# Kernel tuning notes

Hardware: AMD Instinct MI355X
Metric: run time of the kernel (lower is better)

Reference implementation:

```python
import jax, jax.numpy as jnp
import numpy as np

LN_EPS = 1e-5

def _ln(x, g, b):
    m = x.mean(-1, keepdims=True)
    v = jnp.mean((x - m) ** 2, axis=-1, keepdims=True)
    return (x - m) * jax.lax.rsqrt(v + LN_EPS) * g + b


def setup_inputs() -> dict:
    key = jax.random.key(0)
    ks = jax.random.split(key, 8)
    B, S, H = 8, 4096, 2048
    V, L, E = 32, 8, 64   # vocab_size, symbol seq_len, embedding_dim
    sc = 0.02
    d = {}
    d["hidden_states"] = jax.random.normal(ks[0], (B, S, H), jnp.float32)
    # uniform in (0,1) for Gumbel noise: g = -log(-log(u))
    d["gumbel_u"] = jax.random.uniform(ks[1], (B, L, V), jnp.float32, 1e-6, 1.0 - 1e-6)
    d["enc_w1"] = jax.random.normal(ks[2], (256, H), jnp.float32) * sc
    d["enc_b1"] = jnp.zeros((256,), jnp.float32)
    d["ln1_g"] = jnp.ones((256,), jnp.float32)
    d["ln1_b"] = jnp.zeros((256,), jnp.float32)
    d["enc_w2"] = jax.random.normal(ks[3], (L * V, 256), jnp.float32) * sc
    d["enc_b2"] = jnp.zeros((L * V,), jnp.float32)
    d["embed"] = jax.random.normal(ks[4], (V, E), jnp.float32) * sc
    d["dec_w1"] = jax.random.normal(ks[5], (256, L * E), jnp.float32) * sc
    d["dec_b1"] = jnp.zeros((256,), jnp.float32)
    d["ln2_g"] = jnp.ones((256,), jnp.float32)
    d["ln2_b"] = jnp.zeros((256,), jnp.float32)
    d["dec_w2"] = jax.random.normal(ks[6], (H, 256), jnp.float32) * sc
    d["dec_b2"] = jnp.zeros((H,), jnp.float32)
    return d


def reference(hidden_states, gumbel_u, enc_w1, enc_b1, ln1_g, ln1_b, enc_w2, enc_b2,
              embed, dec_w1, dec_b1, ln2_g, ln2_b, dec_w2, dec_b2):
    V, L, TAU = 32, 8, 1.0
    B, S, H = hidden_states.shape
    E = embed.shape[1]
    # encode: mean-pool over sequence, then MLP -> logits [B, L, V]
    pooled = hidden_states.mean(axis=1)
    h = _ln(pooled @ enc_w1.T + enc_b1, ln1_g, ln1_b)
    h = jax.nn.gelu(h, approximate=False)
    logits = (h @ enc_w2.T + enc_b2).reshape(B, L, V)
    # gumbel-softmax with straight-through (hard) estimator
    g = -jnp.log(-jnp.log(gumbel_u))
    y_soft = jax.nn.softmax((logits + g) / TAU, axis=-1)
    idx = jnp.argmax(y_soft, axis=-1)
    y_hard = jax.nn.one_hot(idx, V, dtype=y_soft.dtype)
    soft_symbols = y_hard - jax.lax.stop_gradient(y_soft) + y_soft
    # decode: embed symbols, flatten, MLP back to hidden size
    emb = jnp.einsum('blv,ve->ble', soft_symbols, embed).reshape(B, L * E)
    dh = _ln(emb @ dec_w1.T + dec_b1, ln2_g, ln2_b)
    dh = jax.nn.gelu(dh, approximate=False)
    decoded = dh @ dec_w2.T + dec_b2            # [B, H]
    # residual + 0.1 * broadcast over sequence
    return hidden_states + 0.1 * decoded[:, None, :]
```

## Files before the change

### kernel.cpp

```cpp
#include <hip/hip_runtime.h>
#include <math.h>

#define B 8
#define S 4096
#define H 2048
#define VOC 32
#define LSYM 8
#define EMB 64

typedef float f32x4 __attribute__((ext_vector_type(4)));

__global__ __launch_bounds__(256) void pool_partial(const float* __restrict__ hid,
                                                    float* __restrict__ part,
                                                    int chunk) {
    const int sp = blockIdx.x;
    const int b  = blockIdx.y;
    const int t  = threadIdx.x;
    const float* slab = hid + (size_t)b * S * H + (size_t)sp * chunk * H;
    const int iters = chunk * (H / 1024);
    float4 a0 = {0.f, 0.f, 0.f, 0.f};
    float4 a1 = {0.f, 0.f, 0.f, 0.f};
    for (int i = 0; i < iters; i += 2) {
        const float4 v0 = *reinterpret_cast<const float4*>(slab + (size_t)i * 1024 + t * 4);
        const float4 v1 = *reinterpret_cast<const float4*>(slab + (size_t)(i + 1) * 1024 + t * 4);
        a0.x += v0.x; a0.y += v0.y; a0.z += v0.z; a0.w += v0.w;
        a1.x += v1.x; a1.y += v1.y; a1.z += v1.z; a1.w += v1.w;
    }
    float* dst = part + ((size_t)sp * B + b) * H;
    *reinterpret_cast<float4*>(dst + t * 4)        = a0;
    *reinterpret_cast<float4*>(dst + 1024 + t * 4) = a1;
}

__global__ __launch_bounds__(256) void pool_reduce(const float* __restrict__ part,
                                                   float* __restrict__ pooled,
                                                   int split) {
    const int i4 = blockIdx.x * 256 + threadIdx.x;
    if (i4 >= B * H / 4) return;
    float4 acc = {0.f, 0.f, 0.f, 0.f};
    for (int sp = 0; sp < split; ++sp) {
        const float4 v = *reinterpret_cast<const float4*>(part + (size_t)sp * B * H + (size_t)i4 * 4);
        acc.x += v.x; acc.y += v.y; acc.z += v.z; acc.w += v.w;
    }
    const float inv = 1.0f / (float)S;
    acc.x *= inv; acc.y *= inv; acc.z *= inv; acc.w *= inv;
    *reinterpret_cast<float4*>(pooled + (size_t)i4 * 4) = acc;
}

__global__ __launch_bounds__(256) void enc1_matvec(const float* __restrict__ pooled,
                                                   const float* __restrict__ ew1,
                                                   const float* __restrict__ eb1,
                                                   float* __restrict__ out1) {
    const int wv   = (blockIdx.x * 256 + threadIdx.x) >> 6;
    const int lane = threadIdx.x & 63;
    const int b = wv >> 8, t = wv & 255;
    const float4* wrow = reinterpret_cast<const float4*>(ew1 + (size_t)t * H);
    const float4* prow = reinterpret_cast<const float4*>(pooled + b * H);
    float acc = 0.f;
#pragma unroll
    for (int i = 0; i < 8; ++i) {
        const float4 w = wrow[lane + 64 * i];
        const float4 p = prow[lane + 64 * i];
        acc += w.x * p.x + w.y * p.y + w.z * p.z + w.w * p.w;
    }
    for (int off = 32; off; off >>= 1) acc += __shfl_xor(acc, off, 64);
    if (lane == 0) out1[b * 256 + t] = acc + eb1[t];
}

__device__ __forceinline__ float block_sum256(float x, float* red) {
    const int t = threadIdx.x;
    red[t] = x;
    __syncthreads();
    for (int s = 128; s > 0; s >>= 1) {
        if (t < s) red[t] += red[t + s];
        __syncthreads();
    }
    const float r = red[0];
    __syncthreads();
    return r;
}

__global__ __launch_bounds__(256) void mlp_middle(
    const float* __restrict__ out1, const float* __restrict__ gu,
    const float* __restrict__ g1,  const float* __restrict__ bb1,
    const float* __restrict__ ew2, const float* __restrict__ eb2,
    const float* __restrict__ emb_tab,
    const float* __restrict__ dw1, const float* __restrict__ db1,
    const float* __restrict__ g2,  const float* __restrict__ bb2,
    float* __restrict__ hs2) {
    __shared__ float red[256];
    __shared__ float hs[256];
    __shared__ float es[LSYM * EMB];

    const int b = blockIdx.x;
    const int t = threadIdx.x;

    float acc = out1[b * 256 + t];
    {
        const float m = block_sum256(acc, red) * (1.0f / 256.0f);
        const float d = acc - m;
        const float v = block_sum256(d * d, red) * (1.0f / 256.0f);
        float x = d * rsqrtf(v + 1e-5f) * g1[t] + bb1[t];
        x = 0.5f * x * (1.0f + erff(x * 0.70710678118654752f));
        hs[t] = x;
    }
    __syncthreads();

    float z;
    {
        float a2 = eb2[t];
        const float* w2row = ew2 + t * 256;
        for (int k = 0; k < 256; k += 4) {
            const float4 w = *reinterpret_cast<const float4*>(w2row + k);
            a2 += w.x * hs[k] + w.y * hs[k + 1] + w.z * hs[k + 2] + w.w * hs[k + 3];
        }
        const float u = gu[b * 256 + t];
        z = a2 - logf(-logf(u));
    }

    {
        int   bi = t & 31;
        float bz = z;
        for (int off = 16; off; off >>= 1) {
            const float oz = __shfl_xor(bz, off, 32);
            const int   oi = __shfl_xor(bi, off, 32);
            if (oz > bz || (oz == bz && oi < bi)) { bz = oz; bi = oi; }
        }
        const int l = t >> 5, v32 = t & 31;
        es[l * EMB + v32]      = emb_tab[bi * EMB + v32];
        es[l * EMB + 32 + v32] = emb_tab[bi * EMB + 32 + v32];
    }
    __syncthreads();

    float a3 = db1[t];
    {
        const float* d1row = dw1 + t * (LSYM * EMB);
        for (int k = 0; k < LSYM * EMB; k += 4) {
            const float4 w = *reinterpret_cast<const float4*>(d1row + k);
            a3 += w.x * es[k] + w.y * es[k + 1] + w.z * es[k + 2] + w.w * es[k + 3];
        }
    }
    {
        const float m2 = block_sum256(a3, red) * (1.0f / 256.0f);
        const float dd = a3 - m2;
        const float vv = block_sum256(dd * dd, red) * (1.0f / 256.0f);
        float y = dd * rsqrtf(vv + 1e-5f) * g2[t] + bb2[t];
        y = 0.5f * y * (1.0f + erff(y * 0.70710678118654752f));
        hs2[b * 256 + t] = y;
    }
}

__global__ __launch_bounds__(256) void dec2_matvec(const float* __restrict__ hs2,
                                                   const float* __restrict__ dw2,
                                                   const float* __restrict__ db2,
                                                   float* __restrict__ dec_sc) {
    const int wv   = (blockIdx.x * 256 + threadIdx.x) >> 6;
    const int lane = threadIdx.x & 63;
    const int b = wv >> 11, j = wv & 2047;
    const float4 w = reinterpret_cast<const float4*>(dw2 + (size_t)j * 256)[lane];
    const float4 h = reinterpret_cast<const float4*>(hs2 + b * 256)[lane];
    float acc = w.x * h.x + w.y * h.y + w.z * h.z + w.w * h.w;
    for (int off = 32; off; off >>= 1) acc += __shfl_xor(acc, off, 64);
    if (lane == 0) dec_sc[b * 2048 + j] = 0.1f * (acc + db2[j]);
}

__global__ __launch_bounds__(256) void residual_add(const float* __restrict__ hid,
                                                    const float* __restrict__ dec,
                                                    float* __restrict__ out,
                                                    size_t n4) {
    size_t i = (size_t)blockIdx.x * blockDim.x + threadIdx.x;
    const size_t stride = (size_t)gridDim.x * blockDim.x;
    const float4* __restrict__ hv4 = reinterpret_cast<const float4*>(hid);
    const float4* __restrict__ dv4 = reinterpret_cast<const float4*>(dec);
    f32x4* __restrict__ ov4 = reinterpret_cast<f32x4*>(out);
    for (; i < n4; i += stride) {
        const float4 hv = hv4[i];
        const size_t b  = i >> 21;
        const size_t h4 = i & (H / 4 - 1);
        const float4 dv = dv4[b * (H / 4) + h4];
        f32x4 o;
        o.x = hv.x + dv.x; o.y = hv.y + dv.y; o.z = hv.z + dv.z; o.w = hv.w + dv.w;
        __builtin_nontemporal_store(o, &ov4[i]);
    }
}

extern "C" void kernel_launch(void* const* d_in, const int* in_sizes, int n_in,
                              void* d_out, int out_size, void* d_ws, size_t ws_size,
                              hipStream_t stream) {
    const float* hid   = (const float*)d_in[0];
    const float* gu    = (const float*)d_in[1];
    const float* ew1   = (const float*)d_in[2];
    const float* eb1   = (const float*)d_in[3];
    const float* g1    = (const float*)d_in[4];
    const float* bb1   = (const float*)d_in[5];
    const float* ew2   = (const float*)d_in[6];
    const float* eb2   = (const float*)d_in[7];
    const float* emb   = (const float*)d_in[8];
    const float* dw1   = (const float*)d_in[9];
    const float* db1   = (const float*)d_in[10];
    const float* g2    = (const float*)d_in[11];
    const float* bb2   = (const float*)d_in[12];
    const float* dw2   = (const float*)d_in[13];
    const float* db2   = (const float*)d_in[14];
    float* out = (float*)d_out;

    const size_t avail_floats = ws_size / 4;
    int split = 128;
    while (split > 1 && (size_t)(split + 3) * B * H > avail_floats) split >>= 1;
    const int chunk = S / split;

    float* part   = (float*)d_ws;
    float* pooled = part + (size_t)split * B * H;
    float* dec_sc = pooled + (size_t)B * H;
    float* out1   = dec_sc + (size_t)B * H;
    float* hs2    = out1 + (size_t)B * 256;

    pool_partial<<<dim3(split, B), 256, 0, stream>>>(hid, part, chunk);
    pool_reduce<<<(B * H / 4 + 255) / 256, 256, 0, stream>>>(part, pooled, split);
    enc1_matvec<<<B * 256 / 4, 256, 0, stream>>>(pooled, ew1, eb1, out1);
    mlp_middle<<<B, 256, 0, stream>>>(out1, gu, g1, bb1, ew2, eb2, emb,
                                      dw1, db1, g2, bb2, hs2);
    dec2_matvec<<<B * 2048 / 4, 256, 0, stream>>>(hs2, dw2, db2, dec_sc);
    const size_t n4 = (size_t)B * S * H / 4;
    residual_add<<<2048, 256, 0, stream>>>(hid, dec_sc, out, n4);
}
```

Before: 219.3 us.

## Fuse middle MLP stages into one cooperative kernel with grid syncs

The change merges pool_reduce, enc1_matvec, mlp_middle and dec2_matvec into one cooperative kernel of 256 blocks, separated by grid.sync, which cuts four launches down to one. It fixes the split at 128 with no workspace-size check. The residual_add loop now runs a fixed 32 iterations per thread with one dec load per batch and uses plain stores instead of nontemporal ones. The risks are the cost of each grid-wide sync, a possible workspace overflow, and losing the cache benefit of nontemporal stores.

```diff
diff --git a/kernel.cpp b/kernel.cpp
--- a/kernel.cpp
+++ b/kernel.cpp
@@ -1,23 +1,24 @@
 #include <hip/hip_runtime.h>
+#include <hip/hip_cooperative_groups.h>
 #include <math.h>
+
+namespace cg = cooperative_groups;
 
 #define B 8
 #define S 4096
 #define H 2048
-#define VOC 32
 #define LSYM 8
 #define EMB 64
-
-typedef float f32x4 __attribute__((ext_vector_type(4)));
+#define SPLIT 128
+#define CHUNK (S / SPLIT)
 
 __global__ __launch_bounds__(256) void pool_partial(const float* __restrict__ hid,
-                                                    float* __restrict__ part,
-                                                    int chunk) {
+                                                    float* __restrict__ part) {
     const int sp = blockIdx.x;
     const int b  = blockIdx.y;
     const int t  = threadIdx.x;
-    const float* slab = hid + (size_t)b * S * H + (size_t)sp * chunk * H;
-    const int iters = chunk * (H / 1024);
+    const float* slab = hid + (size_t)b * S * H + (size_t)sp * CHUNK * H;
+    const int iters = CHUNK * (H / 1024);
     float4 a0 = {0.f, 0.f, 0.f, 0.f};
     float4 a1 = {0.f, 0.f, 0.f, 0.f};
     for (int i = 0; i < iters; i += 2) {
@@ -31,40 +32,17 @@
     *reinterpret_cast<float4*>(dst + 1024 + t * 4) = a1;
 }
 
-__global__ __launch_bounds__(256) void pool_reduce(const float* __restrict__ part,
-                                                   float* __restrict__ pooled,
-                                                   int split) {
-    const int i4 = blockIdx.x * 256 + threadIdx.x;
-    if (i4 >= B * H / 4) return;
-    float4 acc = {0.f, 0.f, 0.f, 0.f};
-    for (int sp = 0; sp < split; ++sp) {
-        const float4 v = *reinterpret_cast<const float4*>(part + (size_t)sp * B * H + (size_t)i4 * 4);
-        acc.x += v.x; acc.y += v.y; acc.z += v.z; acc.w += v.w;
-    }
-    const float inv = 1.0f / (float)S;
-    acc.x *= inv; acc.y *= inv; acc.z *= inv; acc.w *= inv;
-    *reinterpret_cast<float4*>(pooled + (size_t)i4 * 4) = acc;
-}
-
-__global__ __launch_bounds__(256) void enc1_matvec(const float* __restrict__ pooled,
-                                                   const float* __restrict__ ew1,
-                                                   const float* __restrict__ eb1,
-                                                   float* __restrict__ out1) {
-    const int wv   = (blockIdx.x * 256 + threadIdx.x) >> 6;
-    const int lane = threadIdx.x & 63;
-    const int b = wv >> 8, t = wv & 255;
-    const float4* wrow = reinterpret_cast<const float4*>(ew1 + (size_t)t * H);
-    const float4* prow = reinterpret_cast<const float4*>(pooled + b * H);
-    float acc = 0.f;
-#pragma unroll
-    for (int i = 0; i < 8; ++i) {
-        const float4 w = wrow[lane + 64 * i];
-        const float4 p = prow[lane + 64 * i];
-        acc += w.x * p.x + w.y * p.y + w.z * p.z + w.w * p.w;
-    }
-    for (int off = 32; off; off >>= 1) acc += __shfl_xor(acc, off, 64);
-    if (lane == 0) out1[b * 256 + t] = acc + eb1[t];
-}
+struct MlpParams {
+    const float* part; const float* gu;
+    const float* ew1; const float* eb1;
+    const float* g1;  const float* bb1;
+    const float* ew2; const float* eb2;
+    const float* emb_tab;
+    const float* dw1; const float* db1;
+    const float* g2;  const float* bb2;
+    const float* dw2; const float* db2;
+    float* pooled; float* out1; float* hs2; float* dec_sc;
+};
 
 __device__ __forceinline__ float block_sum256(float x, float* red) {
     const int t = threadIdx.x;
@@ -79,147 +57,177 @@
     return r;
 }
 
-__global__ __launch_bounds__(256) void mlp_middle(
-    const float* __restrict__ out1, const float* __restrict__ gu,
-    const float* __restrict__ g1,  const float* __restrict__ bb1,
-    const float* __restrict__ ew2, const float* __restrict__ eb2,
-    const float* __restrict__ emb_tab,
-    const float* __restrict__ dw1, const float* __restrict__ db1,
-    const float* __restrict__ g2,  const float* __restrict__ bb2,
-    float* __restrict__ hs2) {
+__global__ __launch_bounds__(256) void mlp_coop(MlpParams p) {
+    cg::grid_group grid = cg::this_grid();
     __shared__ float red[256];
-    __shared__ float hs[256];
+    __shared__ float hsm[256];
     __shared__ float es[LSYM * EMB];
 
-    const int b = blockIdx.x;
-    const int t = threadIdx.x;
-
-    float acc = out1[b * 256 + t];
+    const int bid  = blockIdx.x;
+    const int t    = threadIdx.x;
+    const int gtid = bid * 256 + t;
+    const int wv   = gtid >> 6;
+    const int lane = t & 63;
+
+    if (gtid < B * H / 4) {
+        const float4* pp = reinterpret_cast<const float4*>(p.part);
+        float4 acc = {0.f, 0.f, 0.f, 0.f};
+        for (int sp = 0; sp < SPLIT; ++sp) {
+            const float4 v = pp[(size_t)sp * (B * H / 4) + gtid];
+            acc.x += v.x; acc.y += v.y; acc.z += v.z; acc.w += v.w;
+        }
+        const float inv = 1.0f / (float)S;
+        acc.x *= inv; acc.y *= inv; acc.z *= inv; acc.w *= inv;
+        reinterpret_cast<float4*>(p.pooled)[gtid] = acc;
+    }
+    grid.sync();
+
+#pragma unroll
+    for (int k = 0; k < 2; ++k) {
+        const int o  = wv * 2 + k;
+        const int b  = o >> 8, tt = o & 255;
+        const float4* wrow = reinterpret_cast<const float4*>(p.ew1 + (size_t)tt * H);
+        const float4* prow = reinterpret_cast<const float4*>(p.pooled + b * H);
+        float acc = 0.f;
+#pragma unroll
+        for (int i = 0; i < 8; ++i) {
+            const float4 w = wrow[lane + 64 * i];
+            const float4 v = prow[lane + 64 * i];
+            acc += w.x * v.x + w.y * v.y + w.z * v.z + w.w * v.w;
+        }
+        for (int off = 32; off; off >>= 1) acc += __shfl_xor(acc, off, 64);
+        if (lane == 0) p.out1[o] = acc + p.eb1[tt];
+    }
+    grid.sync();
+
+    if (bid < B) {
+        const int b = bid;
+        float acc = p.out1[b * 256 + t];
+        {
+            const float m = block_sum256(acc, red) * (1.0f / 256.0f);
+            const float d = acc - m;
+            const float v = block_sum256(d * d, red) * (1.0f / 256.0f);
+            float x = d * rsqrtf(v + 1e-5f) * p.g1[t] + p.bb1[t];
+            x = 0.5f * x * (1.0f + erff(x * 0.70710678118654752f));
+            hsm[t] = x;
+        }
+        __syncthreads();
+
+        float z;
+        {
+            float a2 = p.eb2[t];
+            const float* w2row = p.ew2 + t * 256;
+            for (int k = 0; k < 256; k += 4) {
+                const float4 w = *reinterpret_cast<const float4*>(w2row + k);
+                a2 += w.x * hsm[k] + w.y * hsm[k + 1] + w.z * hsm[k + 2] + w.w * hsm[k + 3];
+            }
+            const float u = p.gu[b * 256 + t];
+            z = a2 - logf(-logf(u));
+        }
+        {
+            int   bi = t & 31;
+            float bz = z;
+            for (int off = 16; off; off >>= 1) {
+                const float oz = __shfl_xor(bz, off, 32);
+                const int   oi = __shfl_xor(bi, off, 32);
+                if (oz > bz || (oz == bz && oi < bi)) { bz = oz; bi = oi; }
+            }
+            const int l = t >> 5, v32 = t & 31;
+            es[l * EMB + v32]      = p.emb_tab[bi * EMB + v32];
+            es[l * EMB + 32 + v32] = p.emb_tab[bi * EMB + 32 + v32];
+        }
+        __syncthreads();
+
+        float a3 = p.db1[t];
+        {
+            const float* d1row = p.dw1 + t * (LSYM * EMB);
+            for (int k = 0; k < LSYM * EMB; k += 4) {
+                const float4 w = *reinterpret_cast<const float4*>(d1row + k);
+                a3 += w.x * es[k] + w.y * es[k + 1] + w.z * es[k + 2] + w.w * es[k + 3];
+            }
+        }
+        {
+            const float m2 = block_sum256(a3, red) * (1.0f / 256.0f);
+            const float dd = a3 - m2;
+            const float vv = block_sum256(dd * dd, red) * (1.0f / 256.0f);
+            float y = dd * rsqrtf(vv + 1e-5f) * p.g2[t] + p.bb2[t];
+            y = 0.5f * y * (1.0f + erff(y * 0.70710678118654752f));
+            p.hs2[b * 256 + t] = y;
+        }
+    }
+    grid.sync();
+
     {
-        const float m = block_sum256(acc, red) * (1.0f / 256.0f);
-        const float d = acc - m;
-        const float v = block_sum256(d * d, red) * (1.0f / 256.0f);
-        float x = d * rsqrtf(v + 1e-5f) * g1[t] + bb1[t];
-        x = 0.5f * x * (1.0f + erff(x * 0.70710678118654752f));
-        hs[t] = x;
-    }
-    __syncthreads();
-
-    float z;
-    {
-        float a2 = eb2[t];
-        const float* w2row = ew2 + t * 256;
-        for (int k = 0; k < 256; k += 4) {
-            const float4 w = *reinterpret_cast<const float4*>(w2row + k);
-            a2 += w.x * hs[k] + w.y * hs[k + 1] + w.z * hs[k + 2] + w.w * hs[k + 3];
-        }
-        const float u = gu[b * 256 + t];
-        z = a2 - logf(-logf(u));
-    }
-
-    {
-        int   bi = t & 31;
-        float bz = z;
-        for (int off = 16; off; off >>= 1) {
-            const float oz = __shfl_xor(bz, off, 32);
-            const int   oi = __shfl_xor(bi, off, 32);
-            if (oz > bz || (oz == bz && oi < bi)) { bz = oz; bi = oi; }
-        }
-        const int l = t >> 5, v32 = t & 31;
-        es[l * EMB + v32]      = emb_tab[bi * EMB + v32];
-        es[l * EMB + 32 + v32] = emb_tab[bi * EMB + 32 + v32];
-    }
-    __syncthreads();
-
-    float a3 = db1[t];
-    {
-        const float* d1row = dw1 + t * (LSYM * EMB);
-        for (int k = 0; k < LSYM * EMB; k += 4) {
-            const float4 w = *reinterpret_cast<const float4*>(d1row + k);
-            a3 += w.x * es[k] + w.y * es[k + 1] + w.z * es[k + 2] + w.w * es[k + 3];
-        }
-    }
-    {
-        const float m2 = block_sum256(a3, red) * (1.0f / 256.0f);
-        const float dd = a3 - m2;
-        const float vv = block_sum256(dd * dd, red) * (1.0f / 256.0f);
-        float y = dd * rsqrtf(vv + 1e-5f) * g2[t] + bb2[t];
-        y = 0.5f * y * (1.0f + erff(y * 0.70710678118654752f));
-        hs2[b * 256 + t] = y;
-    }
-}
-
-__global__ __launch_bounds__(256) void dec2_matvec(const float* __restrict__ hs2,
-                                                   const float* __restrict__ dw2,
-                                                   const float* __restrict__ db2,
-                                                   float* __restrict__ dec_sc) {
-    const int wv   = (blockIdx.x * 256 + threadIdx.x) >> 6;
-    const int lane = threadIdx.x & 63;
-    const int b = wv >> 11, j = wv & 2047;
-    const float4 w = reinterpret_cast<const float4*>(dw2 + (size_t)j * 256)[lane];
-    const float4 h = reinterpret_cast<const float4*>(hs2 + b * 256)[lane];
-    float acc = w.x * h.x + w.y * h.y + w.z * h.z + w.w * h.w;
-    for (int off = 32; off; off >>= 1) acc += __shfl_xor(acc, off, 64);
-    if (lane == 0) dec_sc[b * 2048 + j] = 0.1f * (acc + db2[j]);
+        const int base = wv * 16;
+        const int b    = base >> 11;
+        const float4 h = reinterpret_cast<const float4*>(p.hs2 + b * 256)[lane];
+#pragma unroll
+        for (int k = 0; k < 16; ++k) {
+            const int o = base + k, j = o & 2047;
+            const float4 w = reinterpret_cast<const float4*>(p.dw2 + (size_t)j * 256)[lane];
+            float acc = w.x * h.x + w.y * h.y + w.z * h.z + w.w * h.w;
+            for (int off = 32; off; off >>= 1) acc += __shfl_xor(acc, off, 64);
+            if (lane == 0) p.dec_sc[o] = 0.1f * (acc + p.db2[j]);
+        }
+    }
 }
 
 __global__ __launch_bounds__(256) void residual_add(const float* __restrict__ hid,
                                                     const float* __restrict__ dec,
-                                                    float* __restrict__ out,
-                                                    size_t n4) {
-    size_t i = (size_t)blockIdx.x * blockDim.x + threadIdx.x;
-    const size_t stride = (size_t)gridDim.x * blockDim.x;
+                                                    float* __restrict__ out) {
+    const size_t tid0 = (size_t)blockIdx.x * 256 + threadIdx.x;
+    const int h4 = (int)(tid0 & (H / 4 - 1));
     const float4* __restrict__ hv4 = reinterpret_cast<const float4*>(hid);
     const float4* __restrict__ dv4 = reinterpret_cast<const float4*>(dec);
-    f32x4* __restrict__ ov4 = reinterpret_cast<f32x4*>(out);
-    for (; i < n4; i += stride) {
-        const float4 hv = hv4[i];
-        const size_t b  = i >> 21;
-        const size_t h4 = i & (H / 4 - 1);
+    float4* __restrict__ ov4 = reinterpret_cast<float4*>(out);
+    size_t i = tid0;
+#pragma unroll
+    for (int b = 0; b < B; ++b) {
         const float4 dv = dv4[b * (H / 4) + h4];
-        f32x4 o;
-        o.x = hv.x + dv.x; o.y = hv.y + dv.y; o.z = hv.z + dv.z; o.w = hv.w + dv.w;
-        __builtin_nontemporal_store(o, &ov4[i]);
+#pragma unroll
+        for (int r = 0; r < 4; ++r, i += (size_t)1 << 19) {
+            const float4 hv = hv4[i];
+            float4 o;
+            o.x = hv.x + dv.x; o.y = hv.y + dv.y; o.z = hv.z + dv.z; o.w = hv.w + dv.w;
+            ov4[i] = o;
+        }
     }
 }
 
 extern "C" void kernel_launch(void* const* d_in, const int* in_sizes, int n_in,
                               void* d_out, int out_size, void* d_ws, size_t ws_size,
                               hipStream_t stream) {
-    const float* hid   = (const float*)d_in[0];
-    const float* gu    = (const float*)d_in[1];
-    const float* ew1   = (const float*)d_in[2];
-    const float* eb1   = (const float*)d_in[3];
-    const float* g1    = (const float*)d_in[4];
-    const float* bb1   = (const float*)d_in[5];
-    const float* ew2   = (const float*)d_in[6];
-    const float* eb2   = (const float*)d_in[7];
-    const float* emb   = (const float*)d_in[8];
-    const float* dw1   = (const float*)d_in[9];
-    const float* db1   = (const float*)d_in[10];
-    const float* g2    = (const float*)d_in[11];
-    const float* bb2   = (const float*)d_in[12];
-    const float* dw2   = (const float*)d_in[13];
-    const float* db2   = (const float*)d_in[14];
+    const float* hid = (const float*)d_in[0];
     float* out = (float*)d_out;
 
-    const size_t avail_floats = ws_size / 4;
-    int split = 128;
-    while (split > 1 && (size_t)(split + 3) * B * H > avail_floats) split >>= 1;
-    const int chunk = S / split;
-
     float* part   = (float*)d_ws;
-    float* pooled = part + (size_t)split * B * H;
+    float* pooled = part + (size_t)SPLIT * B * H;
     float* dec_sc = pooled + (size_t)B * H;
     float* out1   = dec_sc + (size_t)B * H;
     float* hs2    = out1 + (size_t)B * 256;
 
-    pool_partial<<<dim3(split, B), 256, 0, stream>>>(hid, part, chunk);
-    pool_reduce<<<(B * H / 4 + 255) / 256, 256, 0, stream>>>(part, pooled, split);
-    enc1_matvec<<<B * 256 / 4, 256, 0, stream>>>(pooled, ew1, eb1, out1);
-    mlp_middle<<<B, 256, 0, stream>>>(out1, gu, g1, bb1, ew2, eb2, emb,
-                                      dw1, db1, g2, bb2, hs2);
-    dec2_matvec<<<B * 2048 / 4, 256, 0, stream>>>(hs2, dw2, db2, dec_sc);
-    const size_t n4 = (size_t)B * S * H / 4;
-    residual_add<<<2048, 256, 0, stream>>>(hid, dec_sc, out, n4);
-}
+    pool_partial<<<dim3(SPLIT, B), 256, 0, stream>>>(hid, part);
+
+    MlpParams mp;
+    mp.part = part;
+    mp.gu   = (const float*)d_in[1];
+    mp.ew1  = (const float*)d_in[2];
+    mp.eb1  = (const float*)d_in[3];
+    mp.g1   = (const float*)d_in[4];
+    mp.bb1  = (const float*)d_in[5];
+    mp.ew2  = (const float*)d_in[6];
+    mp.eb2  = (const float*)d_in[7];
+    mp.emb_tab = (const float*)d_in[8];
+    mp.dw1  = (const float*)d_in[9];
+    mp.db1  = (const float*)d_in[10];
+    mp.g2   = (const float*)d_in[11];
+    mp.bb2  = (const float*)d_in[12];
+    mp.dw2  = (const float*)d_in[13];
+    mp.db2  = (const float*)d_in[14];
+    mp.pooled = pooled; mp.out1 = out1; mp.hs2 = hs2; mp.dec_sc = dec_sc;
+
+    void* kargs[] = { (void*)&mp };
+    hipLaunchCooperativeKernel((const void*)mlp_coop, dim3(256), dim3(256), kargs, 0, stream);
+
+    residual_add<<<2048, 256, 0, stream>>>(hid, dec_sc, out);
+}
```

Measured after the change: 292.2 us. 33.2% more time.
